# Kernel optimization log

Measured on AMD Instinct MI355X. Metric: run time of the kernel, lower is better.

Reference implementation:

```python
import jax, jax.numpy as jnp
import numpy as np

B, S, D, H, L = 64, 256, 1024, 1024, 2  # input_size == hidden_size required by the module


def _lstm_params(key, in_dim, hid, scale=0.05):
    k1, k2, k3, k4 = jax.random.split(key, 4)
    return (
        jax.random.normal(k1, (4 * hid, in_dim), jnp.float32) * scale,  # W_ih
        jax.random.normal(k2, (4 * hid, hid), jnp.float32) * scale,     # W_hh
        jax.random.normal(k3, (4 * hid,), jnp.float32) * scale,         # b_ih
        jax.random.normal(k4, (4 * hid,), jnp.float32) * scale,         # b_hh
    )


def setup_inputs() -> dict:
    key = jax.random.key(0)
    ks = jax.random.split(key, 5)
    x = jax.random.normal(ks[0], (B, S, D), jnp.float32)
    inp = {"x": x}
    # encoder: LSTM(input_size=D, hidden_size=H, num_layers=L)
    for l, k in enumerate(jax.random.split(ks[1], L)):
        Wih, Whh, bih, bhh = _lstm_params(k, D if l == 0 else H, H)
        inp[f"enc_Wih{l}"], inp[f"enc_Whh{l}"] = Wih, Whh
        inp[f"enc_bih{l}"], inp[f"enc_bhh{l}"] = bih, bhh
    # decoder: LSTM(input_size=H, hidden_size=D, num_layers=L)
    for l, k in enumerate(jax.random.split(ks[2], L)):
        Wih, Whh, bih, bhh = _lstm_params(k, H if l == 0 else D, D)
        inp[f"dec_Wih{l}"], inp[f"dec_Whh{l}"] = Wih, Whh
        inp[f"dec_bih{l}"], inp[f"dec_bhh{l}"] = bih, bhh
    return inp


def _run_lstm(xs, h0, c0, layers):
    """Stacked LSTM over time. xs: [B,S,Din]; h0,c0: [L,B,Hl]. PyTorch gate order i,f,g,o."""
    def step(carry, x_t):
        h, c = carry  # each [L,B,Hl]
        inp = x_t
        new_h, new_c = [], []
        for l, (Wih, Whh, bih, bhh) in enumerate(layers):
            gates = inp @ Wih.T + h[l] @ Whh.T + (bih + bhh)  # [B,4H]
            i, f, g, o = jnp.split(gates, 4, axis=-1)
            c_l = jax.nn.sigmoid(f) * c[l] + jax.nn.sigmoid(i) * jnp.tanh(g)
            h_l = jax.nn.sigmoid(o) * jnp.tanh(c_l)
            new_h.append(h_l)
            new_c.append(c_l)
            inp = h_l
        return (jnp.stack(new_h), jnp.stack(new_c)), inp
    (h_n, c_n), ys = jax.lax.scan(step, (h0, c0), jnp.swapaxes(xs, 0, 1))
    return jnp.swapaxes(ys, 0, 1), h_n, c_n  # ys: [B,S,Hl]


def reference(x,
              enc_Wih0, enc_Whh0, enc_bih0, enc_bhh0,
              enc_Wih1, enc_Whh1, enc_bih1, enc_bhh1,
              dec_Wih0, dec_Whh0, dec_bih0, dec_bhh0,
              dec_Wih1, dec_Whh1, dec_bih1, dec_bhh1):
    enc_layers = [(enc_Wih0, enc_Whh0, enc_bih0, enc_bhh0),
                  (enc_Wih1, enc_Whh1, enc_bih1, enc_bhh1)]
    dec_layers = [(dec_Wih0, dec_Whh0, dec_bih0, dec_bhh0),
                  (dec_Wih1, dec_Whh1, dec_bih1, dec_bhh1)]
    b = x.shape[0]
    z = jnp.zeros((L, b, H), x.dtype)
    # encode
    _, h_n, c_n = _run_lstm(x, z, z, enc_layers)
    emb = h_n[L - 1]  # [B,H]
    # decode: flip feature dim, teacher-forced inputs [emb, flipped_x[:, :-1]]
    flipped_x = jnp.flip(x, axis=2)
    dec_in = jnp.concatenate([emb[:, None, :], flipped_x[:, :-1]], axis=1)  # [B,S,H]
    dec_out, _, _ = _run_lstm(dec_in, h_n, c_n, dec_layers)  # [B,S,D]
    decoded = jnp.flip(dec_out, axis=2)
    return emb, decoded
```

## Files before the change

### kernel.cpp

```cpp
#include <hip/hip_runtime.h>
#include <hip/hip_fp16.h>


#define NBLK 256
#define NTHR 256
#define LDS_BYTES (128 * 1024)
#define HS 65536

typedef _Float16 half8 __attribute__((ext_vector_type(8)));
typedef float    f32x4 __attribute__((ext_vector_type(4)));

__device__ __forceinline__ float sigm_(float x) { return 1.f / (1.f + __expf(-x)); }
__device__ __forceinline__ float tanh_(float x) {
  float e = __expf(-2.f * fabsf(x));
  float r = (1.f - e) / (1.f + e);
  return x >= 0.f ? r : -r;
}

__global__ __launch_bounds__(256) void cvt_x(const float* __restrict__ src,
                                             __half* __restrict__ dst, int n) {
  int i = blockIdx.x * 256 + threadIdx.x;
  if (i < n) dst[i] = __float2half(src[i]);
}

__global__ void fail_mark(float* out, float ws_mb) { out[0] = 1.0e6f * ws_mb; }

__device__ __forceinline__ void issue8c(const __half* p,
    half8& r0, half8& r1, half8& r2, half8& r3,
    half8& r4, half8& r5, half8& r6, half8& r7) {
  asm volatile(
    "global_load_dwordx4 %0, %8, off sc0 sc1\n\t"
    "global_load_dwordx4 %1, %8, off offset:64 sc0 sc1\n\t"
    "global_load_dwordx4 %2, %8, off offset:128 sc0 sc1\n\t"
    "global_load_dwordx4 %3, %8, off offset:192 sc0 sc1\n\t"
    "global_load_dwordx4 %4, %8, off offset:256 sc0 sc1\n\t"
    "global_load_dwordx4 %5, %8, off offset:320 sc0 sc1\n\t"
    "global_load_dwordx4 %6, %8, off offset:384 sc0 sc1\n\t"
    "global_load_dwordx4 %7, %8, off offset:448 sc0 sc1"
    : "=&v"(r0), "=&v"(r1), "=&v"(r2), "=&v"(r3),
      "=&v"(r4), "=&v"(r5), "=&v"(r6), "=&v"(r7)
    : "v"(p) : "memory");
}
__device__ __forceinline__ void issue8p(const __half* p,
    half8& r0, half8& r1, half8& r2, half8& r3,
    half8& r4, half8& r5, half8& r6, half8& r7) {
  asm volatile(
    "global_load_dwordx4 %0, %8, off\n\t"
    "global_load_dwordx4 %1, %8, off offset:64\n\t"
    "global_load_dwordx4 %2, %8, off offset:128\n\t"
    "global_load_dwordx4 %3, %8, off offset:192\n\t"
    "global_load_dwordx4 %4, %8, off offset:256\n\t"
    "global_load_dwordx4 %5, %8, off offset:320\n\t"
    "global_load_dwordx4 %6, %8, off offset:384\n\t"
    "global_load_dwordx4 %7, %8, off offset:448"
    : "=&v"(r0), "=&v"(r1), "=&v"(r2), "=&v"(r3),
      "=&v"(r4), "=&v"(r5), "=&v"(r6), "=&v"(r7)
    : "v"(p) : "memory");
}

__device__ __forceinline__ void st2_coh(__half* p, float h) {
  unsigned v = (unsigned)__half_as_ushort(__float2half(h));
  asm volatile("global_store_short %0, %1, off sc0 sc1" :: "v"(p), "v"(v) : "memory");
}

__device__ __forceinline__ void poll16(const unsigned* c, unsigned& sA, unsigned& sB) {
  unsigned a0,a1,a2,a3,a4,a5,a6,a7, b0,b1,b2,b3,b4,b5,b6,b7;
  const unsigned* c2 = c + 1024;
  asm volatile(
    "global_load_dword %0, %16, off sc0 sc1\n\t"
    "global_load_dword %1, %16, off offset:64 sc0 sc1\n\t"
    "global_load_dword %2, %16, off offset:128 sc0 sc1\n\t"
    "global_load_dword %3, %16, off offset:192 sc0 sc1\n\t"
    "global_load_dword %4, %16, off offset:256 sc0 sc1\n\t"
    "global_load_dword %5, %16, off offset:320 sc0 sc1\n\t"
    "global_load_dword %6, %16, off offset:384 sc0 sc1\n\t"
    "global_load_dword %7, %16, off offset:448 sc0 sc1\n\t"
    "global_load_dword %8, %17, off sc0 sc1\n\t"
    "global_load_dword %9, %17, off offset:64 sc0 sc1\n\t"
    "global_load_dword %10, %17, off offset:128 sc0 sc1\n\t"
    "global_load_dword %11, %17, off offset:192 sc0 sc1\n\t"
    "global_load_dword %12, %17, off offset:256 sc0 sc1\n\t"
    "global_load_dword %13, %17, off offset:320 sc0 sc1\n\t"
    "global_load_dword %14, %17, off offset:384 sc0 sc1\n\t"
    "global_load_dword %15, %17, off offset:448 sc0 sc1\n\t"
    "s_waitcnt vmcnt(0)"
    : "=&v"(a0), "=&v"(a1), "=&v"(a2), "=&v"(a3),
      "=&v"(a4), "=&v"(a5), "=&v"(a6), "=&v"(a7),
      "=&v"(b0), "=&v"(b1), "=&v"(b2), "=&v"(b3),
      "=&v"(b4), "=&v"(b5), "=&v"(b6), "=&v"(b7)
    : "v"(c), "v"(c2) : "memory");
  sA = a0 + a1 + a2 + a3 + a4 + a5 + a6 + a7;
  sB = b0 + b1 + b2 + b3 + b4 + b5 + b6 + b7;
}

#define WAITVM(n) do { asm volatile("s_waitcnt vmcnt(" #n ")" ::: "memory"); \
                       __builtin_amdgcn_sched_barrier(0); } while (0)
#define DRAIN()   asm volatile("s_waitcnt vmcnt(0)" ::: "memory")
#define BANK(X) X##0, X##1, X##2, X##3, X##4, X##5, X##6, X##7
#define ISSUE(X, c) do { const __half* _p = ((c) < 4 ? pa + (c) * 256 : pb + ((c) - 4) * 256); \
                         if (((c) >= 4) && coh1) issue8c(_p, BANK(X)); \
                         else issue8p(_p, BANK(X)); } while (0)
#define MFMA16(X, c) do { const __half* _b = ldsb + (c) * 8192; \
  accA = __builtin_amdgcn_mfma_f32_16x16x32_f16(X##0, *(const half8*)(_b + 0*1024), accA, 0,0,0); \
  accB = __builtin_amdgcn_mfma_f32_16x16x32_f16(X##0, *(const half8*)(_b + 0*1024 + 128), accB, 0,0,0); \
  accA = __builtin_amdgcn_mfma_f32_16x16x32_f16(X##1, *(const half8*)(_b + 1*1024), accA, 0,0,0); \
  accB = __builtin_amdgcn_mfma_f32_16x16x32_f16(X##1, *(const half8*)(_b + 1*1024 + 128), accB, 0,0,0); \
  accA = __builtin_amdgcn_mfma_f32_16x16x32_f16(X##2, *(const half8*)(_b + 2*1024), accA, 0,0,0); \
  accB = __builtin_amdgcn_mfma_f32_16x16x32_f16(X##2, *(const half8*)(_b + 2*1024 + 128), accB, 0,0,0); \
  accA = __builtin_amdgcn_mfma_f32_16x16x32_f16(X##3, *(const half8*)(_b + 3*1024), accA, 0,0,0); \
  accB = __builtin_amdgcn_mfma_f32_16x16x32_f16(X##3, *(const half8*)(_b + 3*1024 + 128), accB, 0,0,0); \
  accA = __builtin_amdgcn_mfma_f32_16x16x32_f16(X##4, *(const half8*)(_b + 4*1024), accA, 0,0,0); \
  accB = __builtin_amdgcn_mfma_f32_16x16x32_f16(X##4, *(const half8*)(_b + 4*1024 + 128), accB, 0,0,0); \
  accA = __builtin_amdgcn_mfma_f32_16x16x32_f16(X##5, *(const half8*)(_b + 5*1024), accA, 0,0,0); \
  accB = __builtin_amdgcn_mfma_f32_16x16x32_f16(X##5, *(const half8*)(_b + 5*1024 + 128), accB, 0,0,0); \
  accA = __builtin_amdgcn_mfma_f32_16x16x32_f16(X##6, *(const half8*)(_b + 6*1024), accA, 0,0,0); \
  accB = __builtin_amdgcn_mfma_f32_16x16x32_f16(X##6, *(const half8*)(_b + 6*1024 + 128), accB, 0,0,0); \
  accA = __builtin_amdgcn_mfma_f32_16x16x32_f16(X##7, *(const half8*)(_b + 7*1024), accA, 0,0,0); \
  accB = __builtin_amdgcn_mfma_f32_16x16x32_f16(X##7, *(const half8*)(_b + 7*1024 + 128), accB, 0,0,0); \
  } while (0)

#define PIPE_GENERIC() do { \
  ISSUE(A, 0); ISSUE(B, 1); ISSUE(C, 2); ISSUE(D, 3); \
  WAITVM(24); MFMA16(A, 0); ISSUE(A, 4); \
  WAITVM(24); MFMA16(B, 1); ISSUE(B, 5); \
  WAITVM(24); MFMA16(C, 2); ISSUE(C, 6); \
  WAITVM(24); MFMA16(D, 3); ISSUE(D, 7); \
  WAITVM(24); MFMA16(A, 4); \
  WAITVM(16); MFMA16(B, 5); \
  WAITVM(8);  MFMA16(C, 6); \
  WAITVM(0);  MFMA16(D, 7); \
} while (0)

#define PIPE_PF() do { \
  ISSUE(A, 2); ISSUE(B, 3); ISSUE(C, 4); ISSUE(D, 5); \
  MFMA16(E, 0); MFMA16(F, 1); \
  WAITVM(24); MFMA16(A, 2); ISSUE(A, 6); \
  WAITVM(24); MFMA16(B, 3); ISSUE(B, 7); \
  WAITVM(16); MFMA16(C, 4); \
  WAITVM(8);  MFMA16(D, 5); \
  WAITVM(8);  MFMA16(A, 6); \
  WAITVM(0);  MFMA16(B, 7); \
} while (0)

#define PREFETCH_EF(ptr) do { issue8p((ptr), BANK(E)); issue8p((ptr) + 256, BANK(F)); } while (0)

#define EPI(ACC, CST, BB, NIDX) do { \
  _Pragma("unroll") \
  for (int r = 0; r < 4; ++r) { \
    float v = ACC[r] + (BB); \
    float vx4  = __shfl_xor(v, 4); \
    float vx8  = __shfl_xor(v, 8); \
    float vx12 = __shfl_xor(vx4, 8); \
    float vi = gi == 0 ? v    : gi == 1 ? vx4  : gi == 2 ? vx8  : vx12; \
    float vf = gi == 0 ? vx4  : gi == 1 ? v    : gi == 2 ? vx12 : vx8; \
    float vg = gi == 0 ? vx8  : gi == 1 ? vx12 : gi == 2 ? v    : vx4; \
    float vo = gi == 0 ? vx12 : gi == 1 ? vx8  : gi == 2 ? vx4  : v; \
    float cn = sigm_(vf) * CST[r] + sigm_(vi) * tanh_(vg); \
    CST[r] = cn; \
    float h = sigm_(vo) * tanh_(cn); \
    if (gi == 0) { \
      const int b = mtile * 16 + kq * 4 + r; \
      const int j = jb * 8 + (NIDX) * 4 + (lane & 3); \
      st2_coh(hdst + (size_t)b * 1024 + j, h); \
      if (layer == 1) { \
        if (seg == 0) { if (p == 256) { \
            out[(size_t)b * 1024 + j] = h; \
            st2_coh(femb + (size_t)b * 1024 + (1023 - j), h); } \
        } else { \
          out[65536 + ((size_t)b * 256 + (p - 1)) * 1024 + (1023 - j)] = h; } \
      } \
    } \
  } } while (0)

__global__ __launch_bounds__(256, 1) void lstm_persist(
    const __half* __restrict__ xf16,
    const float* __restrict__ eWih0, const float* __restrict__ eWhh0,
    const float* __restrict__ eWih1, const float* __restrict__ eWhh1,
    const float* __restrict__ dWih0, const float* __restrict__ dWhh0,
    const float* __restrict__ dWih1, const float* __restrict__ dWhh1,
    const float* __restrict__ ebi0, const float* __restrict__ ebh0,
    const float* __restrict__ ebi1, const float* __restrict__ ebh1,
    const float* __restrict__ dbi0, const float* __restrict__ dbh0,
    const float* __restrict__ dbi1, const float* __restrict__ dbh1,
    __half* __restrict__ hE0,
    __half* __restrict__ hD0,
    __half* __restrict__ h1pp,
    __half* __restrict__ femb, float* __restrict__ out,
    unsigned* __restrict__ ctr) {
  extern __shared__ __half lds[];
  const int tid   = threadIdx.x, lane = tid & 63;
  const int mtile = tid >> 6;
  const int layer = blockIdx.x >> 7;
  const int jb    = blockIdx.x & 127;
  const int c4 = lane & 15, kq = lane >> 4;
  const int gi = c4 >> 2;
  const int arow = mtile * 16 + c4;
  unsigned* myarr = ctr + (layer ? 1024 : 0) + (blockIdx.x & 7) * 16;
  const int coh1 = (layer == 1);

  f32x4 cA = {0.f, 0.f, 0.f, 0.f};
  f32x4 cB = {0.f, 0.f, 0.f, 0.f};

  for (int seg = 0; seg < 2; ++seg) {
    const float* Wih; const float* Whh; int flip = 0;
    if (seg == 0) { Wih = layer ? eWih1 : eWih0; Whh = layer ? eWhh1 : eWhh0; }
    else { Wih = layer ? dWih1 : dWih0; Whh = layer ? dWhh1 : dWhh0; flip = (layer == 0); }
    const int k0 = tid * 8;
    for (int i = 0; i < 32; ++i) {
      int cc4 = i & 15, ct = i >> 4;
      int n = (cc4 >> 2) * 1024 + jb * 8 + ct * 4 + (cc4 & 3);
      half8 t;
      if (k0 < 1024) {
        if (flip) {
          #pragma unroll
          for (int e = 0; e < 8; ++e) t[e] = (_Float16)Wih[(size_t)n * 1024 + 1023 - k0 - e];
        } else {
          #pragma unroll
          for (int e = 0; e < 8; ++e) t[e] = (_Float16)Wih[(size_t)n * 1024 + k0 + e];
        }
      } else {
        #pragma unroll
        for (int e = 0; e < 8; ++e) t[e] = (_Float16)Whh[(size_t)n * 1024 + k0 - 1024 + e];
      }
      *(half8*)(lds + ((size_t)tid * 32 + i) * 8) = t;
    }
    const float* bi = (seg == 0) ? (layer ? ebi1 : ebi0) : (layer ? dbi1 : dbi0);
    const float* bh = (seg == 0) ? (layer ? ebh1 : ebh0) : (layer ? dbh1 : dbh0);
    const int nl0 = gi * 1024 + jb * 8 + (lane & 3);
    const float bb0 = bi[nl0] + bh[nl0];
    const float bb1 = bi[nl0 + 4] + bh[nl0 + 4];
    __syncthreads();
    DRAIN();

    const __half* ldsb = lds + ((size_t)kq * 32 + c4) * 8;
    __half* h0b = seg ? hD0 : hE0;

    half8 A0,A1,A2,A3,A4,A5,A6,A7, B0,B1,B2,B3,B4,B5,B6,B7,
          C0,C1,C2,C3,C4,C5,C6,C7, D0,D1,D2,D3,D4,D5,D6,D7,
          E0,E1,E2,E3,E4,E5,E6,E7, F0,F1,F2,F3,F4,F5,F6,F7;
    int havepf = 0;

    for (int p = 0; p <= 256; ++p) {
      const unsigned T  = (unsigned)(seg * 257 + p) * 128u;
      const unsigned tA = T;
      const unsigned tB = (layer == 1) ? T
                         : ((seg == 1 && p == 0) ? 257u * 128u : 0u);
      if (tid == 0 && (tA | tB)) {
        unsigned sA, sB;
        int g = 0;
        for (;;) {
          poll16(ctr, sA, sB);
          if (sA >= tA && sB >= tB) break;
          __builtin_amdgcn_s_sleep(1);
          if (++g > (1 << 18)) break;
        }
      }
      __syncthreads();

      const int active = (layer == 0) ? (p <= 255) : (p >= 1);
      if (active) {
        const __half* l0rec = (seg && p == 0) ? hE0 + (size_t)256 * HS
                                              : h0b + (size_t)p * HS;
        const __half* l1in  = h0b + (size_t)p * HS;
        const __half* l1rec = h1pp + (size_t)((p + 1) & 1) * HS;
        const __half* s1 = (layer == 0) ? l0rec : l1rec;
        const __half* s0;
        long long st0;
        if (layer == 0) {
          if (seg == 0)      { s0 = xf16 + (size_t)p * 1024;       st0 = 262144; }
          else if (p == 0)   { s0 = femb;                          st0 = 1024;   }
          else               { s0 = xf16 + (size_t)(p - 1) * 1024; st0 = 262144; }
        } else             { s0 = l1in;                            st0 = 1024;   }

        const __half* pa = s0 + (long long)arow * st0 + kq * 8;
        const __half* pb = s1 + (long long)arow * 1024 + kq * 8;
        f32x4 accA = {0.f, 0.f, 0.f, 0.f};
        f32x4 accB = {0.f, 0.f, 0.f, 0.f};
        if (havepf) PIPE_PF(); else PIPE_GENERIC();

        __half* hdst = (layer == 0) ? h0b + (size_t)(p + 1) * HS
                                    : h1pp + (size_t)(p & 1) * HS;
        EPI(accA, cA, bb0, 0);
        EPI(accB, cB, bb1, 1);
      }

      havepf = 0;
      if (layer == 0 && p < 255) {
        const __half* ns0 = (seg == 0) ? xf16 + (size_t)(p + 1) * 1024
                                       : xf16 + (size_t)p * 1024;
        const __half* npa = ns0 + (long long)arow * 262144 + kq * 8;
        PREFETCH_EF(npa);
        havepf = 1;
      }

      DRAIN();
      __syncthreads();
      if (tid == 0)
        __hip_atomic_fetch_add(myarr, 1u, __ATOMIC_RELAXED, __HIP_MEMORY_SCOPE_AGENT);
    }
    __syncthreads();
  }
}

extern "C" void kernel_launch(void* const* d_in, const int* in_sizes, int n_in,
                              void* d_out, int out_size, void* d_ws, size_t ws_size,
                              hipStream_t stream) {
  const float* x     = (const float*)d_in[0];
  const float* eWih0 = (const float*)d_in[1];
  const float* eWhh0 = (const float*)d_in[2];
  const float* ebih0 = (const float*)d_in[3];
  const float* ebhh0 = (const float*)d_in[4];
  const float* eWih1 = (const float*)d_in[5];
  const float* eWhh1 = (const float*)d_in[6];
  const float* ebih1 = (const float*)d_in[7];
  const float* ebhh1 = (const float*)d_in[8];
  const float* dWih0 = (const float*)d_in[9];
  const float* dWhh0 = (const float*)d_in[10];
  const float* dbih0 = (const float*)d_in[11];
  const float* dbhh0 = (const float*)d_in[12];
  const float* dWih1 = (const float*)d_in[13];
  const float* dWhh1 = (const float*)d_in[14];
  const float* dbih1 = (const float*)d_in[15];
  const float* dbhh1 = (const float*)d_in[16];
  float* out = (float*)d_out;

  char* ws = (char*)d_ws;
  size_t off = 0;
  auto alloc = [&](size_t bytes) { char* p = ws + off; off += (bytes + 255) & ~(size_t)255; return p; };
  const size_t SLOT = (size_t)HS * sizeof(__half);
  __half* xf16 = (__half*)alloc((size_t)64 * 256 * 1024 * sizeof(__half));
  __half* hE0  = (__half*)alloc(257 * SLOT);
  __half* hD0  = (__half*)alloc(257 * SLOT);
  __half* h1pp = (__half*)alloc(2 * SLOT);
  __half* femb = (__half*)alloc(SLOT);
  unsigned* ctr = (unsigned*)alloc(8192);

  if (ws_size < off) {
    hipLaunchKernelGGL(fail_mark, dim3(1), dim3(1), 0, stream,
                       out, (float)(ws_size >> 20));
    return;
  }

  const int xn = 64 * 256 * 1024;
  cvt_x<<<(xn + 255) / 256, 256, 0, stream>>>(x, xf16, xn);

  hipMemsetAsync(hE0, 0, SLOT, stream);
  hipMemsetAsync(h1pp, 0, SLOT, stream);
  hipMemsetAsync(ctr, 0, 8192, stream);

  hipFuncSetAttribute((const void*)lstm_persist,
                      hipFuncAttributeMaxDynamicSharedMemorySize, LDS_BYTES);
  lstm_persist<<<NBLK, NTHR, LDS_BYTES, stream>>>(
      xf16,
      eWih0, eWhh0, eWih1, eWhh1, dWih0, dWhh0, dWih1, dWhh1,
      ebih0, ebhh0, ebih1, ebhh1, dbih0, dbhh0, dbih1, dbhh1,
      hE0, hD0, h1pp, femb, out, ctr);
}
```

Before: 6.748 ms.

## Replace atomic counter barrier with per-block flags, packed h stores, full-history layer-1 buffers

Inter-block synchronisation moves from atomic increments on 8 shared counters (polled by one thread) to one monotonically increasing flag per block, written with a coherent store and polled by a whole wavefront using __all. Hidden-state outputs are packed via shuffles into 8-byte coherent stores instead of per-element 2-byte stores. Layer-1 hidden states get a full per-timestep history buffer when workspace allows, so layer-1 loads can use the non-coherent path instead of reusing a ping-pong buffer. The flag store also moves ahead of the next-step prefetch issue. This targets barrier latency and store traffic, at the cost of more workspace and more wave-wide polling loads.

```diff
diff --git a/kernel.cpp b/kernel.cpp
--- a/kernel.cpp
+++ b/kernel.cpp
@@ -9,6 +9,7 @@
 
 typedef _Float16 half8 __attribute__((ext_vector_type(8)));
 typedef float    f32x4 __attribute__((ext_vector_type(4)));
+typedef unsigned uint32x2 __attribute__((ext_vector_type(2)));
 
 __device__ __forceinline__ float sigm_(float x) { return 1.f / (1.f + __expf(-x)); }
 __device__ __forceinline__ float tanh_(float x) {
@@ -58,39 +59,24 @@
     : "v"(p) : "memory");
 }
 
-__device__ __forceinline__ void st2_coh(__half* p, float h) {
-  unsigned v = (unsigned)__half_as_ushort(__float2half(h));
-  asm volatile("global_store_short %0, %1, off sc0 sc1" :: "v"(p), "v"(v) : "memory");
-}
-
-__device__ __forceinline__ void poll16(const unsigned* c, unsigned& sA, unsigned& sB) {
-  unsigned a0,a1,a2,a3,a4,a5,a6,a7, b0,b1,b2,b3,b4,b5,b6,b7;
-  const unsigned* c2 = c + 1024;
+__device__ __forceinline__ void st8_coh(__half* p, uint32x2 v) {
+  asm volatile("global_store_dwordx2 %0, %1, off sc0 sc1" :: "v"(p), "v"(v) : "memory");
+}
+__device__ __forceinline__ void flag_store(unsigned* p, unsigned v) {
+  asm volatile("global_store_dword %0, %1, off sc0 sc1" :: "v"(p), "v"(v) : "memory");
+}
+__device__ __forceinline__ void poll4(const unsigned* c, int lane,
+    unsigned& f0, unsigned& f1, unsigned& g0, unsigned& g1) {
+  const unsigned* p0 = c + lane;
+  const unsigned* p1 = c + 1024 + lane;
   asm volatile(
-    "global_load_dword %0, %16, off sc0 sc1\n\t"
-    "global_load_dword %1, %16, off offset:64 sc0 sc1\n\t"
-    "global_load_dword %2, %16, off offset:128 sc0 sc1\n\t"
-    "global_load_dword %3, %16, off offset:192 sc0 sc1\n\t"
-    "global_load_dword %4, %16, off offset:256 sc0 sc1\n\t"
-    "global_load_dword %5, %16, off offset:320 sc0 sc1\n\t"
-    "global_load_dword %6, %16, off offset:384 sc0 sc1\n\t"
-    "global_load_dword %7, %16, off offset:448 sc0 sc1\n\t"
-    "global_load_dword %8, %17, off sc0 sc1\n\t"
-    "global_load_dword %9, %17, off offset:64 sc0 sc1\n\t"
-    "global_load_dword %10, %17, off offset:128 sc0 sc1\n\t"
-    "global_load_dword %11, %17, off offset:192 sc0 sc1\n\t"
-    "global_load_dword %12, %17, off offset:256 sc0 sc1\n\t"
-    "global_load_dword %13, %17, off offset:320 sc0 sc1\n\t"
-    "global_load_dword %14, %17, off offset:384 sc0 sc1\n\t"
-    "global_load_dword %15, %17, off offset:448 sc0 sc1\n\t"
+    "global_load_dword %0, %4, off sc0 sc1\n\t"
+    "global_load_dword %1, %4, off offset:256 sc0 sc1\n\t"
+    "global_load_dword %2, %5, off sc0 sc1\n\t"
+    "global_load_dword %3, %5, off offset:256 sc0 sc1\n\t"
     "s_waitcnt vmcnt(0)"
-    : "=&v"(a0), "=&v"(a1), "=&v"(a2), "=&v"(a3),
-      "=&v"(a4), "=&v"(a5), "=&v"(a6), "=&v"(a7),
-      "=&v"(b0), "=&v"(b1), "=&v"(b2), "=&v"(b3),
-      "=&v"(b4), "=&v"(b5), "=&v"(b6), "=&v"(b7)
-    : "v"(c), "v"(c2) : "memory");
-  sA = a0 + a1 + a2 + a3 + a4 + a5 + a6 + a7;
-  sB = b0 + b1 + b2 + b3 + b4 + b5 + b6 + b7;
+    : "=&v"(f0), "=&v"(f1), "=&v"(g0), "=&v"(g1)
+    : "v"(p0), "v"(p1) : "memory");
 }
 
 #define WAITVM(n) do { asm volatile("s_waitcnt vmcnt(" #n ")" ::: "memory"); \
@@ -145,6 +131,7 @@
 #define PREFETCH_EF(ptr) do { issue8p((ptr), BANK(E)); issue8p((ptr) + 256, BANK(F)); } while (0)
 
 #define EPI(ACC, CST, BB, NIDX) do { \
+  const int J0 = jb * 8 + (NIDX) * 4; \
   _Pragma("unroll") \
   for (int r = 0; r < 4; ++r) { \
     float v = ACC[r] + (BB); \
@@ -158,16 +145,28 @@
     float cn = sigm_(vf) * CST[r] + sigm_(vi) * tanh_(vg); \
     CST[r] = cn; \
     float h = sigm_(vo) * tanh_(cn); \
-    if (gi == 0) { \
-      const int b = mtile * 16 + kq * 4 + r; \
-      const int j = jb * 8 + (NIDX) * 4 + (lane & 3); \
-      st2_coh(hdst + (size_t)b * 1024 + j, h); \
-      if (layer == 1) { \
-        if (seg == 0) { if (p == 256) { \
-            out[(size_t)b * 1024 + j] = h; \
-            st2_coh(femb + (size_t)b * 1024 + (1023 - j), h); } \
-        } else { \
-          out[65536 + ((size_t)b * 256 + (p - 1)) * 1024 + (1023 - j)] = h; } \
+    const int b = mtile * 16 + kq * 4 + r; \
+    int hu = (int)__half_as_ushort(__float2half(h)); \
+    int qb = lane & ~3; \
+    int v0 = __shfl(hu, qb), v1 = __shfl(hu, qb + 1); \
+    int v2 = __shfl(hu, qb + 2), v3 = __shfl(hu, qb + 3); \
+    if (c4 == 0) { \
+      uint32x2 pk = { (unsigned)(v0 & 0xffff) | ((unsigned)v1 << 16), \
+                      (unsigned)(v2 & 0xffff) | ((unsigned)v3 << 16) }; \
+      st8_coh(hdst + (size_t)b * 1024 + J0, pk); \
+    } \
+    if (layer == 1) { \
+      if (seg == 0) { \
+        if (p == 256) { \
+          if (gi == 0) out[(size_t)b * 1024 + J0 + (lane & 3)] = h; \
+          if (c4 == 0) { \
+            uint32x2 pr = { (unsigned)(v3 & 0xffff) | ((unsigned)v2 << 16), \
+                            (unsigned)(v1 & 0xffff) | ((unsigned)v0 << 16) }; \
+            st8_coh(femb + (size_t)b * 1024 + (1020 - J0), pr); \
+          } \
+        } \
+      } else { \
+        if (gi == 0) out[65536 + ((size_t)b * 256 + (p - 1)) * 1024 + (1023 - (J0 + (lane & 3)))] = h; \
       } \
     } \
   } } while (0)
@@ -182,21 +181,21 @@
     const float* __restrict__ ebi1, const float* __restrict__ ebh1,
     const float* __restrict__ dbi0, const float* __restrict__ dbh0,
     const float* __restrict__ dbi1, const float* __restrict__ dbh1,
-    __half* __restrict__ hE0,
-    __half* __restrict__ hD0,
+    __half* __restrict__ hE0, __half* __restrict__ hD0,
+    __half* __restrict__ hE1, __half* __restrict__ hD1,
     __half* __restrict__ h1pp,
     __half* __restrict__ femb, float* __restrict__ out,
-    unsigned* __restrict__ ctr) {
+    unsigned* __restrict__ ctr, int h1fresh) {
   extern __shared__ __half lds[];
-  const int tid   = threadIdx.x, lane = tid & 63;
-  const int mtile = tid >> 6;
+  const int tid   = threadIdx.x, lane = tid & 63, wid = tid >> 6;
+  const int mtile = wid;
   const int layer = blockIdx.x >> 7;
   const int jb    = blockIdx.x & 127;
   const int c4 = lane & 15, kq = lane >> 4;
   const int gi = c4 >> 2;
   const int arow = mtile * 16 + c4;
-  unsigned* myarr = ctr + (layer ? 1024 : 0) + (blockIdx.x & 7) * 16;
-  const int coh1 = (layer == 1);
+  unsigned* myflag = ctr + (layer ? 1024 : 0) + jb;
+  const int coh1 = (layer == 1) && !h1fresh;
 
   f32x4 cA = {0.f, 0.f, 0.f, 0.f};
   f32x4 cB = {0.f, 0.f, 0.f, 0.f};
@@ -234,6 +233,7 @@
 
     const __half* ldsb = lds + ((size_t)kq * 32 + c4) * 8;
     __half* h0b = seg ? hD0 : hE0;
+    __half* h1b = seg ? hD1 : hE1;
 
     half8 A0,A1,A2,A3,A4,A5,A6,A7, B0,B1,B2,B3,B4,B5,B6,B7,
           C0,C1,C2,C3,C4,C5,C6,C7, D0,D1,D2,D3,D4,D5,D6,D7,
@@ -241,16 +241,17 @@
     int havepf = 0;
 
     for (int p = 0; p <= 256; ++p) {
-      const unsigned T  = (unsigned)(seg * 257 + p) * 128u;
+      const unsigned T  = (unsigned)(seg * 257 + p);
       const unsigned tA = T;
       const unsigned tB = (layer == 1) ? T
-                         : ((seg == 1 && p == 0) ? 257u * 128u : 0u);
-      if (tid == 0 && (tA | tB)) {
-        unsigned sA, sB;
+                         : ((seg == 1 && p == 0) ? 257u : 0u);
+      if (wid == 0 && (tA | tB)) {
         int g = 0;
         for (;;) {
-          poll16(ctr, sA, sB);
-          if (sA >= tA && sB >= tB) break;
+          unsigned f0, f1, g0, g1;
+          poll4(ctr, lane, f0, f1, g0, g1);
+          int ok = (f0 >= tA) && (f1 >= tA) && (g0 >= tB) && (g1 >= tB);
+          if (__all(ok)) break;
           __builtin_amdgcn_s_sleep(1);
           if (++g > (1 << 18)) break;
         }
@@ -262,7 +263,9 @@
         const __half* l0rec = (seg && p == 0) ? hE0 + (size_t)256 * HS
                                               : h0b + (size_t)p * HS;
         const __half* l1in  = h0b + (size_t)p * HS;
-        const __half* l1rec = h1pp + (size_t)((p + 1) & 1) * HS;
+        const __half* l1rec = h1fresh
+            ? ((seg && p == 1) ? hE1 + (size_t)256 * HS : h1b + (size_t)(p - 1) * HS)
+            : h1pp + (size_t)((p + 1) & 1) * HS;
         const __half* s1 = (layer == 0) ? l0rec : l1rec;
         const __half* s0;
         long long st0;
@@ -278,11 +281,16 @@
         f32x4 accB = {0.f, 0.f, 0.f, 0.f};
         if (havepf) PIPE_PF(); else PIPE_GENERIC();
 
-        __half* hdst = (layer == 0) ? h0b + (size_t)(p + 1) * HS
-                                    : h1pp + (size_t)(p & 1) * HS;
+        __half* hdst = (layer == 0)
+            ? h0b + (size_t)(p + 1) * HS
+            : (h1fresh ? h1b + (size_t)p * HS : h1pp + (size_t)(p & 1) * HS);
         EPI(accA, cA, bb0, 0);
         EPI(accB, cB, bb1, 1);
       }
+
+      DRAIN();
+      __syncthreads();
+      if (tid == 0) flag_store(myflag, (unsigned)(seg * 257 + p + 1));
 
       havepf = 0;
       if (layer == 0 && p < 255) {
@@ -292,11 +300,6 @@
         PREFETCH_EF(npa);
         havepf = 1;
       }
-
-      DRAIN();
-      __syncthreads();
-      if (tid == 0)
-        __hip_atomic_fetch_add(myarr, 1u, __ATOMIC_RELAXED, __HIP_MEMORY_SCOPE_AGENT);
     }
     __syncthreads();
   }
@@ -331,21 +334,36 @@
   __half* xf16 = (__half*)alloc((size_t)64 * 256 * 1024 * sizeof(__half));
   __half* hE0  = (__half*)alloc(257 * SLOT);
   __half* hD0  = (__half*)alloc(257 * SLOT);
-  __half* h1pp = (__half*)alloc(2 * SLOT);
-  __half* femb = (__half*)alloc(SLOT);
-  unsigned* ctr = (unsigned*)alloc(8192);
-
+  size_t base_end = off;
+
+  int h1fresh = 1;
+  __half *hE1, *hD1, *h1pp, *femb;
+  unsigned* ctr;
+  hE1 = (__half*)alloc(257 * SLOT);
+  hD1 = (__half*)alloc(257 * SLOT);
+  h1pp = hE1;
+  femb = (__half*)alloc(SLOT);
+  ctr  = (unsigned*)alloc(8192);
   if (ws_size < off) {
-    hipLaunchKernelGGL(fail_mark, dim3(1), dim3(1), 0, stream,
-                       out, (float)(ws_size >> 20));
-    return;
+    h1fresh = 0;
+    off = base_end;
+    h1pp = (__half*)alloc(2 * SLOT);
+    hE1 = h1pp; hD1 = h1pp;
+    femb = (__half*)alloc(SLOT);
+    ctr  = (unsigned*)alloc(8192);
+    if (ws_size < off) {
+      hipLaunchKernelGGL(fail_mark, dim3(1), dim3(1), 0, stream,
+                         out, (float)(ws_size >> 20));
+      return;
+    }
   }
 
   const int xn = 64 * 256 * 1024;
   cvt_x<<<(xn + 255) / 256, 256, 0, stream>>>(x, xf16, xn);
 
   hipMemsetAsync(hE0, 0, SLOT, stream);
-  hipMemsetAsync(h1pp, 0, SLOT, stream);
+  if (h1fresh) hipMemsetAsync(hE1, 0, SLOT, stream);
+  else         hipMemsetAsync(h1pp, 0, SLOT, stream);
   hipMemsetAsync(ctr, 0, 8192, stream);
 
   hipFuncSetAttribute((const void*)lstm_persist,
@@ -354,5 +372,5 @@
       xf16,
       eWih0, eWhh0, eWih1, eWhh1, dWih0, dWhh0, dWih1, dWhh1,
       ebih0, ebhh0, ebih1, ebhh1, dbih0, dbhh0, dbih1, dbhh1,
-      hE0, hD0, h1pp, femb, out, ctr);
-}
+      hE0, hD0, hE1, hD1, h1pp, femb, out, ctr, h1fresh);
+}
```

After: 7.583 ms. 1.12x slower.
